# Kernel tuning notes

Hardware: AMD Instinct MI355X
Metric: run time of the kernel (lower is better)

## Reference

```python
import jax, jax.numpy as jnp
import numpy as np

N = 50000      # nodes
E = 800000     # edges (before self-loops)
DIN = 146      # input feature dim
D = 128        # hidden/out dim
G = 64         # graphs in batch
L = 4          # number of GCNConv layers (len(hidden_dims[1:]) + 1)
NC = 10        # classes
EPS = 1e-5     # BatchNorm eps


def setup_inputs() -> dict:
    key = jax.random.key(0)
    ks = jax.random.split(key, 12)
    x = jax.random.normal(ks[0], (N, DIN), jnp.float32)
    edge_index = jax.random.randint(ks[1], (2, E), 0, N, dtype=jnp.int64)
    batch = jnp.sort(jax.random.randint(ks[2], (N,), 0, G, dtype=jnp.int64))

    def lin(k, shape, fan_in):
        return (jax.random.normal(k, shape, jnp.float32) / np.sqrt(fan_in)).astype(jnp.float32)

    W_emb = lin(ks[3], (DIN, D), DIN)
    b_emb = jnp.zeros((D,), jnp.float32)
    W_gcn = lin(ks[4], (L, D, D), D)
    b_gcn = jnp.zeros((L, D), jnp.float32)
    bn_gamma = jnp.ones((L, D), jnp.float32)
    bn_beta = jnp.zeros((L, D), jnp.float32)
    W_r1 = lin(ks[5], (D, D // 2), D)
    b_r1 = jnp.zeros((D // 2,), jnp.float32)
    W_r2 = lin(ks[6], (D // 2, D // 4), D // 2)
    b_r2 = jnp.zeros((D // 4,), jnp.float32)
    W_r3 = lin(ks[7], (D // 4, NC), D // 4)
    b_r3 = jnp.zeros((NC,), jnp.float32)
    return {"x": x, "edge_index": edge_index, "batch": batch,
            "W_emb": W_emb, "b_emb": b_emb, "W_gcn": W_gcn, "b_gcn": b_gcn,
            "bn_gamma": bn_gamma, "bn_beta": bn_beta,
            "W_r1": W_r1, "b_r1": b_r1, "W_r2": W_r2, "b_r2": b_r2,
            "W_r3": W_r3, "b_r3": b_r3}


def reference(x, edge_index, batch, W_emb, b_emb, W_gcn, b_gcn,
              bn_gamma, bn_beta, W_r1, b_r1, W_r2, b_r2, W_r3, b_r3):
    # gcn_norm with self-loops (fill_value=1, improved=False)
    loop = jnp.arange(N, dtype=edge_index.dtype)
    src = jnp.concatenate([edge_index[0], loop])
    dst = jnp.concatenate([edge_index[1], loop])
    deg = jax.ops.segment_sum(jnp.ones(src.shape, x.dtype), dst, num_segments=N)
    dinv = jax.lax.rsqrt(jnp.maximum(deg, jnp.asarray(1e-12, x.dtype)))  # deg >= 1 (self loops)
    norm = (dinv[src] * dinv[dst])[:, None]  # [E+N, 1]

    h = x @ W_emb + b_emb  # embedding_h
    for l in range(L):
        h_in = h
        m = h @ W_gcn[l]                                            # [N, D]
        h = jax.ops.segment_sum(m[src] * norm, dst, num_segments=N) + b_gcn[l]
        # BatchNorm1d (training-mode batch stats, biased var)
        mu = h.mean(axis=0)
        var = h.var(axis=0)
        h = (h - mu) * jax.lax.rsqrt(var + EPS) * bn_gamma[l] + bn_beta[l]
        h = jax.nn.relu(h)
        h = h_in + h  # residual (dims always match here)

    # global_mean_pool over batch ids
    sums = jax.ops.segment_sum(h, batch, num_segments=G)
    cnts = jax.ops.segment_sum(jnp.ones((N, 1), h.dtype), batch, num_segments=G)
    hg = sums / jnp.maximum(cnts, 1.0)

    # MLPReadout: two hidden layers halving dims, then classifier
    z = jax.nn.relu(hg @ W_r1 + b_r1)
    z = jax.nn.relu(z @ W_r2 + b_r2)
    return z @ W_r3 + b_r3  # [G, NC]
```

## Files before the change

kernel.cpp:

```cpp
#include <hip/hip_runtime.h>
#include <hip/hip_bf16.h>

#define NN 50000
#define EE 800000
#define DIN 146
#define DD 128
#define GG 64
#define LL 4
#define NC 10
#define BN_EPS 1e-5f

#define KP_EMB 160
#define AST_L  136
#define NCOPY 64
#define NPW 4
#define RST 129

#define C_INIT   256
#define C_REPACK (C_INIT + 31250)
#define C_BATCH  (C_REPACK + 196)
#define C_PARAMS (C_BATCH + 384)
#define C_WT     (C_PARAMS + 400)

#define B_EDGE 3125
#define B_TOT  (B_EDGE + 391)
#define S_SCAT 3125
#define S_TOT  (S_SCAT + 391)

typedef __attribute__((ext_vector_type(8))) short bf16x8;
typedef __attribute__((ext_vector_type(4))) float f32x4;

__device__ __forceinline__ float bf2f(__hip_bfloat16 v) { return __bfloat162float(v); }
__device__ __forceinline__ float loadf(const void* p, long i, int f32) {
    return f32 ? ((const float*)p)[i] : bf2f(((const __hip_bfloat16*)p)[i]);
}
__device__ __forceinline__ unsigned short f2bf_bits(float f) {
    __hip_bfloat16 h = __float2bfloat16(f);
    return *(unsigned short*)&h;
}
__device__ __forceinline__ float bfu2f(unsigned short u) {
    return __uint_as_float((unsigned)u << 16);
}
__device__ __forceinline__ void acc_add8(float* acc, uint4 v) {
    acc[0] += __uint_as_float(v.x << 16);
    acc[1] += __uint_as_float(v.x & 0xffff0000u);
    acc[2] += __uint_as_float(v.y << 16);
    acc[3] += __uint_as_float(v.y & 0xffff0000u);
    acc[4] += __uint_as_float(v.z << 16);
    acc[5] += __uint_as_float(v.z & 0xffff0000u);
    acc[6] += __uint_as_float(v.w << 16);
    acc[7] += __uint_as_float(v.w & 0xffff0000u);
}

__global__ void detect_kernel(const void* ei, const void* batch, const void* Wemb,
                              int* __restrict__ flags) {
    __shared__ int s_edge_nz, s_batch_nz, s_f32_cnt;
    int t = threadIdx.x;
    if (t == 0) { s_edge_nz = 0; s_batch_nz = 0; s_f32_cnt = 0; }
    __syncthreads();
    {   const int* w = (const int*)ei;
        long j = ((long)t * ((2L * EE) / 64)) | 1;
        if (w[j] != 0) atomicAdd(&s_edge_nz, 1);
    }
    {   const int* w = (const int*)batch;
        long j = ((long)(NN / 2) + (long)t * ((NN / 2) / 64)) | 1;
        if (j < NN && w[j] != 0) atomicAdd(&s_batch_nz, 1);
    }
    {   const unsigned short* w = (const unsigned short*)Wemb;
        unsigned short v = w[2 * t];
        int ex = (v >> 7) & 0xFF;
        if (v != 0 && ex >= 128) atomicAdd(&s_f32_cnt, 1);
    }
    __syncthreads();
    if (t == 0) {
        flags[0] = (s_edge_nz == 0) ? 1 : 0;
        flags[1] = (s_batch_nz == 0) ? 1 : 0;
        flags[2] = (s_f32_cnt >= 8) ? 1 : 0;
    }
}

struct Param { const void* src; float* dst; int src_n; int dst_n; };
struct Params12 { Param p[12]; };
struct WtDesc { const void* src; long src_off; unsigned short* dst; int K; int Kpad; };
struct WtDescs5 { WtDesc p[5]; };

__global__ __launch_bounds__(256) void mega_conv_kernel(
    const void* __restrict__ x, const void* __restrict__ batch,
    const int* __restrict__ flags, unsigned short* __restrict__ xb,
    int* __restrict__ deg, float* __restrict__ statmulti, float* __restrict__ hgsum,
    int* __restrict__ b32, Params12 P, WtDescs5 W)
{
    int b = blockIdx.x;
    int t = threadIdx.x;
    if (b < C_INIT) {
        int i = b * 256 + t;
        if (i < NN) deg[i] = 0;
        if (i < LL * NCOPY * 256) statmulti[i] = 0.0f;
        if (i < GG * DD) hgsum[i] = 0.0f;
    } else if (b < C_REPACK) {
        int f32 = flags[2];
        long idx = (long)(b - C_INIT) * 256 + t;
        int row = (int)(idx / KP_EMB);
        int k = (int)(idx - (long)row * KP_EMB);
        float v = (k < DIN) ? loadf(x, (long)row * DIN + k, f32) : 0.0f;
        xb[idx] = f2bf_bits(v);
    } else if (b < C_BATCH) {
        int i = (b - C_REPACK) * 256 + t;
        if (i < NN) b32[i] = flags[1] ? ((const int*)batch)[2L * i] : ((const int*)batch)[i];
    } else if (b < C_PARAMS) {
        int f32 = flags[2];
        int bb = b - C_BATCH;
        const Param& e = P.p[bb >> 5];
        int idx = (bb & 31) * 256 + t;
        if (idx < e.dst_n)
            e.dst[idx] = (idx < e.src_n) ? loadf(e.src, idx, f32) : 0.0f;
    } else {
        int f32 = flags[2];
        int bb = b - C_PARAMS;
        int y = bb / 80;
        const WtDesc& e = W.p[y];
        int idx = (bb - y * 80) * 256 + t;
        if (idx < 128 * e.Kpad) {
            int n = idx / e.Kpad, k = idx - n * e.Kpad;
            float v = (k < e.K) ? loadf(e.src, e.src_off + (long)k * DD + n, f32) : 0.0f;
            e.dst[idx] = f2bf_bits(v);
        }
    }
}


__global__ __launch_bounds__(256) void edge_emb_kernel(
    const void* __restrict__ ei, const int* __restrict__ flags,
    int* __restrict__ src32, int* __restrict__ dst32,
    int* __restrict__ rank, int* __restrict__ deg,
    const unsigned short* __restrict__ Ab,
    const unsigned short* __restrict__ Wt,
    const float* __restrict__ bias,
    unsigned short* __restrict__ hb, int n)
{
    int t = threadIdx.x;
    if (blockIdx.x < B_EDGE) {
        int e = blockIdx.x * 256 + t;
        const int* w = (const int*)ei;
        int s, d;
        if (flags[0]) { s = w[2L * e]; d = w[2L * (EE + e)]; }
        else          { s = w[e];      d = w[EE + e]; }
        src32[e] = s; dst32[e] = d;
        int r = 0;
        if ((unsigned)d < (unsigned)NN) r = atomicAdd(&deg[d], 1);
        rank[e] = r;
        return;
    }
    int r0 = (blockIdx.x - B_EDGE) * 128;
    int lane = t & 63, w = t >> 6;
    int m = lane & 15, quad = lane >> 4;
    int rbase = r0 + w * 32;
    bf16x8 a[2][5];
    #pragma unroll
    for (int rt = 0; rt < 2; ++rt)
        #pragma unroll
        for (int c = 0; c < 5; ++c) {
            int rr = rbase + rt * 16 + m; if (rr > n - 1) rr = n - 1;
            a[rt][c] = *(const bf16x8*)(Ab + (long)rr * KP_EMB + c * 32 + quad * 8);
        }
    f32x4 acc[2][8];
    #pragma unroll
    for (int t8 = 0; t8 < 8; ++t8) {
        float bv = bias[t8 * 16 + m];
        f32x4 ai = {bv, bv, bv, bv};
        acc[0][t8] = ai; acc[1][t8] = ai;
    }
    #pragma unroll
    for (int t8 = 0; t8 < 8; ++t8) {
        #pragma unroll
        for (int c = 0; c < 5; ++c) {
            bf16x8 b = *(const bf16x8*)(Wt + (long)(t8 * 16 + m) * KP_EMB + c * 32 + quad * 8);
            acc[0][t8] = __builtin_amdgcn_mfma_f32_16x16x32_bf16(a[0][c], b, acc[0][t8], 0, 0, 0);
            acc[1][t8] = __builtin_amdgcn_mfma_f32_16x16x32_bf16(a[1][c], b, acc[1][t8], 0, 0, 0);
        }
    }
    #pragma unroll
    for (int rt = 0; rt < 2; ++rt)
        #pragma unroll
        for (int t8 = 0; t8 < 8; ++t8)
            #pragma unroll
            for (int rg = 0; rg < 4; ++rg) {
                int row = rbase + rt * 16 + quad * 4 + rg;
                int col = t8 * 16 + m;
                if (row < n) hb[(long)row * DD + col] = f2bf_bits(acc[rt][t8][rg]);
            }
}

__global__ void scan1_kernel(const int* __restrict__ cnt, int* __restrict__ off,
                             int* __restrict__ bsum, float* __restrict__ dinv, int n) {
    int t = threadIdx.x;
    int i = blockIdx.x * 256 + t;
    int v = (i < n) ? cnt[i] : 0;
    if (i < n) dinv[i] = rsqrtf((float)(v + 1));
    int lane = t & 63, w = t >> 6;
    int x = v;
    #pragma unroll
    for (int s = 1; s < 64; s <<= 1) {
        int y = __shfl_up(x, s, 64);
        if (lane >= s) x += y;
    }
    __shared__ int wsum[4];
    if (lane == 63) wsum[w] = x;
    __syncthreads();
    if (t == 0) {
        int a = 0;
        #pragma unroll
        for (int k = 0; k < 4; ++k) { int tmp = wsum[k]; wsum[k] = a; a += tmp; }
        bsum[blockIdx.x] = a;
    }
    __syncthreads();
    int excl = x - v + wsum[w];
    if (i < n) off[i] = excl;
}

__global__ void scan2_kernel(int* __restrict__ bsum, int* __restrict__ boff,
                             int* __restrict__ off_last, int nb) {
    int t = threadIdx.x;
    int v = (t < nb) ? bsum[t] : 0;
    int lane = t & 63, w = t >> 6;
    int x = v;
    #pragma unroll
    for (int s = 1; s < 64; s <<= 1) {
        int y = __shfl_up(x, s, 64);
        if (lane >= s) x += y;
    }
    __shared__ int wsum[4];
    if (lane == 63) wsum[w] = x;
    __syncthreads();
    __shared__ int total_s;
    if (t == 0) {
        int a = 0;
        #pragma unroll
        for (int k = 0; k < 4; ++k) { int tmp = wsum[k]; wsum[k] = a; a += tmp; }
        total_s = a;
    }
    __syncthreads();
    int bval = x - v + wsum[w];
    if (t < nb) boff[t] = bval;
    if (t == nb - 1) *off_last = total_s - bval;
}

__global__ __launch_bounds__(256) void scat_mm_kernel(
    const int* __restrict__ src, const int* __restrict__ dst,
    const int* __restrict__ rank, const int* __restrict__ off,
    const int* __restrict__ boff, int* __restrict__ src_s,
    const unsigned short* __restrict__ Ab,
    const unsigned short* __restrict__ Wt,
    const float* __restrict__ dinv,
    unsigned short* __restrict__ Mb, int n)
{
    int t = threadIdx.x;
    if (blockIdx.x < S_SCAT) {
        int e = blockIdx.x * 256 + t;
        int s = src[e], d = dst[e];
        if ((unsigned)s >= (unsigned)NN || (unsigned)d >= (unsigned)NN) return;
        src_s[off[d] + boff[d >> 8] + rank[e]] = s;
        return;
    }
    int r0 = (blockIdx.x - S_SCAT) * 128;
    int lane = t & 63, w = t >> 6;
    int m = lane & 15, quad = lane >> 4;
    int rbase = r0 + w * 32;
    bf16x8 a[2][4];
    #pragma unroll
    for (int rt = 0; rt < 2; ++rt)
        #pragma unroll
        for (int c = 0; c < 4; ++c) {
            int rr = rbase + rt * 16 + m; if (rr > n - 1) rr = n - 1;
            a[rt][c] = *(const bf16x8*)(Ab + (long)rr * DD + c * 32 + quad * 8);
        }
    float dv[2][4];
    #pragma unroll
    for (int rt = 0; rt < 2; ++rt)
        #pragma unroll
        for (int rg = 0; rg < 4; ++rg) {
            int row = rbase + rt * 16 + quad * 4 + rg; if (row > n - 1) row = n - 1;
            dv[rt][rg] = dinv[row];
        }
    f32x4 acc[2][8];
    #pragma unroll
    for (int t8 = 0; t8 < 8; ++t8) {
        f32x4 z = {0.f, 0.f, 0.f, 0.f};
        acc[0][t8] = z; acc[1][t8] = z;
    }
    #pragma unroll
    for (int t8 = 0; t8 < 8; ++t8) {
        #pragma unroll
        for (int c = 0; c < 4; ++c) {
            bf16x8 b = *(const bf16x8*)(Wt + (long)(t8 * 16 + m) * DD + c * 32 + quad * 8);
            acc[0][t8] = __builtin_amdgcn_mfma_f32_16x16x32_bf16(a[0][c], b, acc[0][t8], 0, 0, 0);
            acc[1][t8] = __builtin_amdgcn_mfma_f32_16x16x32_bf16(a[1][c], b, acc[1][t8], 0, 0, 0);
        }
    }
    #pragma unroll
    for (int rt = 0; rt < 2; ++rt)
        #pragma unroll
        for (int t8 = 0; t8 < 8; ++t8)
            #pragma unroll
            for (int rg = 0; rg < 4; ++rg) {
                int row = rbase + rt * 16 + quad * 4 + rg;
                int col = t8 * 16 + m;
                if (row < n) Mb[(long)row * DD + col] = f2bf_bits(dv[rt][rg] * acc[rt][t8][rg]);
            }
}

__global__ __launch_bounds__(256) void gemm_fused_kernel(
    const unsigned short* __restrict__ aggb, unsigned short* __restrict__ hb,
    const float* __restrict__ statmulti, const float* __restrict__ gamma,
    const float* __restrict__ beta, const float* __restrict__ dinv,
    const unsigned short* __restrict__ Wt, unsigned short* __restrict__ Mb, int n)
{
    __shared__ unsigned short As[128 * AST_L];
    __shared__ float bnsh[256];
    int t = threadIdx.x;
    int r0 = blockIdx.x * 128;
    {
        float s = 0.0f;
        #pragma unroll 8
        for (int k = 0; k < NCOPY; ++k) s += statmulti[k * 256 + t];
        bnsh[t] = s;
    }
    __syncthreads();
    {
        int c4 = (t & 31) * 4, rsub = t >> 5;
        float inv_n = 1.0f / (float)n;
        float4 sm = *(const float4*)&bnsh[c4];
        float4 sq = *(const float4*)&bnsh[128 + c4];
        float4 ga = *(const float4*)&gamma[c4];
        float4 be = *(const float4*)&beta[c4];
        float4 mu, rs;
        mu.x = sm.x * inv_n; mu.y = sm.y * inv_n; mu.z = sm.z * inv_n; mu.w = sm.w * inv_n;
        rs.x = rsqrtf(sq.x * inv_n - mu.x * mu.x + BN_EPS) * ga.x;
        rs.y = rsqrtf(sq.y * inv_n - mu.y * mu.y + BN_EPS) * ga.y;
        rs.z = rsqrtf(sq.z * inv_n - mu.z * mu.z + BN_EPS) * ga.z;
        rs.w = rsqrtf(sq.w * inv_n - mu.w * mu.w + BN_EPS) * ga.w;
        #pragma unroll 4
        for (int i = 0; i < 16; ++i) {
            int row = i * 8 + rsub;
            int r = r0 + row;
            unsigned short o0 = 0, o1 = 0, o2 = 0, o3 = 0;
            if (r < n) {
                long g = (long)r * DD + c4;
                ushort4 au = *(const ushort4*)&aggb[g];
                ushort4 hu = *(const ushort4*)&hb[g];
                float h0 = bfu2f(hu.x) + fmaxf((bfu2f(au.x) - mu.x) * rs.x + be.x, 0.0f);
                float h1 = bfu2f(hu.y) + fmaxf((bfu2f(au.y) - mu.y) * rs.y + be.y, 0.0f);
                float h2 = bfu2f(hu.z) + fmaxf((bfu2f(au.z) - mu.z) * rs.z + be.z, 0.0f);
                float h3 = bfu2f(hu.w) + fmaxf((bfu2f(au.w) - mu.w) * rs.w + be.w, 0.0f);
                o0 = f2bf_bits(h0); o1 = f2bf_bits(h1);
                o2 = f2bf_bits(h2); o3 = f2bf_bits(h3);
                ushort4 ho; ho.x = o0; ho.y = o1; ho.z = o2; ho.w = o3;
                *(ushort4*)&hb[g] = ho;
            }
            unsigned short* dst = &As[row * AST_L + c4];
            dst[0] = o0; dst[1] = o1; dst[2] = o2; dst[3] = o3;
        }
    }
    __syncthreads();
    int lane = t & 63, w = t >> 6;
    int m = lane & 15, quad = lane >> 4;
    int rl = w * 32;
    int rbase = r0 + rl;
    bf16x8 a[2][4];
    #pragma unroll
    for (int rt = 0; rt < 2; ++rt)
        #pragma unroll
        for (int c = 0; c < 4; ++c)
            a[rt][c] = *(const bf16x8*)(As + (rl + rt * 16 + m) * AST_L + c * 32 + quad * 8);
    float dv[2][4];
    #pragma unroll
    for (int rt = 0; rt < 2; ++rt)
        #pragma unroll
        for (int rg = 0; rg < 4; ++rg) {
            int row = rbase + rt * 16 + quad * 4 + rg; if (row > n - 1) row = n - 1;
            dv[rt][rg] = dinv[row];
        }
    f32x4 acc[2][8];
    #pragma unroll
    for (int t8 = 0; t8 < 8; ++t8) {
        f32x4 z = {0.f, 0.f, 0.f, 0.f};
        acc[0][t8] = z; acc[1][t8] = z;
    }
    #pragma unroll
    for (int t8 = 0; t8 < 8; ++t8) {
        #pragma unroll
        for (int c = 0; c < 4; ++c) {
            bf16x8 b = *(const bf16x8*)(Wt + (long)(t8 * 16 + m) * DD + c * 32 + quad * 8);
            acc[0][t8] = __builtin_amdgcn_mfma_f32_16x16x32_bf16(a[0][c], b, acc[0][t8], 0, 0, 0);
            acc[1][t8] = __builtin_amdgcn_mfma_f32_16x16x32_bf16(a[1][c], b, acc[1][t8], 0, 0, 0);
        }
    }
    #pragma unroll
    for (int rt = 0; rt < 2; ++rt)
        #pragma unroll
        for (int t8 = 0; t8 < 8; ++t8)
            #pragma unroll
            for (int rg = 0; rg < 4; ++rg) {
                int row = rbase + rt * 16 + quad * 4 + rg;
                int col = t8 * 16 + m;
                if (row < n) Mb[(long)row * DD + col] = f2bf_bits(dv[rt][rg] * acc[rt][t8][rg]);
            }
}

__global__ __launch_bounds__(256) void agg_kernel(
    const unsigned short* __restrict__ mb, const int* __restrict__ off,
    const int* __restrict__ boff, const int* __restrict__ src_s,
    const float* __restrict__ dinv, const float* __restrict__ bias,
    unsigned short* __restrict__ aggb, float* __restrict__ statacc)
{
    __shared__ float sred[4][4 * RST];
    __shared__ float2 ssum[4][64], ssq[4][64];
    int t = threadIdx.x;
    int wv = t >> 6, lane = t & 63;
    int grp = lane >> 4, sl = lane & 15;
    float* red = sred[wv];
    float2 bi = ((const float2*)bias)[lane];
    float2 sAcc = {0.0f, 0.0f}, qAcc = {0.0f, 0.0f};
    int i0 = (blockIdx.x * 4 + wv) * NPW;
    #pragma unroll 1
    for (int ni = 0; ni < NPW; ++ni) {
        int i = i0 + ni;
        if (i >= NN) break;
        float acc[8];
        #pragma unroll
        for (int k = 0; k < 8; ++k) acc[k] = 0.0f;
        if (grp == 0) {
            uint4 v = *(const uint4*)(mb + (long)i * DD + sl * 8);
            acc_add8(acc, v);
        }
        int e  = off[i] + boff[i >> 8];
        int e1 = off[i + 1] + boff[(i + 1) >> 8];
        for (; e + 16 <= e1; e += 16) {
            int j0 = src_s[e + grp];
            int j1 = src_s[e + 4 + grp];
            int j2 = src_s[e + 8 + grp];
            int j3 = src_s[e + 12 + grp];
            uint4 v0 = *(const uint4*)(mb + (long)j0 * DD + sl * 8);
            uint4 v1 = *(const uint4*)(mb + (long)j1 * DD + sl * 8);
            uint4 v2 = *(const uint4*)(mb + (long)j2 * DD + sl * 8);
            uint4 v3 = *(const uint4*)(mb + (long)j3 * DD + sl * 8);
            acc_add8(acc, v0);
            acc_add8(acc, v1);
            acc_add8(acc, v2);
            acc_add8(acc, v3);
        }
        for (; e + 8 <= e1; e += 8) {
            int ja = src_s[e + grp];
            int jb = src_s[e + 4 + grp];
            uint4 va = *(const uint4*)(mb + (long)ja * DD + sl * 8);
            uint4 vb = *(const uint4*)(mb + (long)jb * DD + sl * 8);
            acc_add8(acc, va);
            acc_add8(acc, vb);
        }
        for (; e + 4 <= e1; e += 4) {
            int j = src_s[e + grp];
            uint4 v = *(const uint4*)(mb + (long)j * DD + sl * 8);
            acc_add8(acc, v);
        }
        if (e + grp < e1) {
            int j = src_s[e + grp];
            uint4 v = *(const uint4*)(mb + (long)j * DD + sl * 8);
            acc_add8(acc, v);
        }
        #pragma unroll
        for (int k = 0; k < 8; ++k) red[grp * RST + sl * 8 + k] = acc[k];
        asm volatile("" ::: "memory");
        float c0 = 0.0f, c1 = 0.0f;
        #pragma unroll
        for (int g = 0; g < 4; ++g) {
            c0 += red[g * RST + 2 * lane];
            c1 += red[g * RST + 2 * lane + 1];
        }
        asm volatile("" ::: "memory");
        float di = dinv[i];
        float o0 = di * c0 + bi.x;
        float o1 = di * c1 + bi.y;
        unsigned packed = ((unsigned)f2bf_bits(o1) << 16) | f2bf_bits(o0);
        ((unsigned*)aggb)[(long)i * 64 + lane] = packed;
        sAcc.x += o0; sAcc.y += o1;
        qAcc.x += o0 * o0; qAcc.y += o1 * o1;
    }
    ssum[wv][lane] = sAcc; ssq[wv][lane] = qAcc;
    __syncthreads();
    if (wv == 0) {
        float2 s0 = ssum[0][lane], s1 = ssum[1][lane], s2 = ssum[2][lane], s3 = ssum[3][lane];
        float2 q0 = ssq[0][lane], q1 = ssq[1][lane], q2 = ssq[2][lane], q3 = ssq[3][lane];
        float sx = s0.x + s1.x + s2.x + s3.x;
        float sy = s0.y + s1.y + s2.y + s3.y;
        float qx = q0.x + q1.x + q2.x + q3.x;
        float qy = q0.y + q1.y + q2.y + q3.y;
        float* copy = statacc + (blockIdx.x & (NCOPY - 1)) * 256;
        atomicAdd(&copy[2 * lane], sx);
        atomicAdd(&copy[2 * lane + 1], sy);
        atomicAdd(&copy[128 + 2 * lane], qx);
        atomicAdd(&copy[128 + 2 * lane + 1], qy);
    }
}

__global__ void pool1_kernel(const unsigned short* __restrict__ hb,
                             const unsigned short* __restrict__ aggb,
                             const float* __restrict__ statmulti,
                             const float* __restrict__ gamma, const float* __restrict__ beta,
                             const int* __restrict__ b32, float* __restrict__ hgsum, int n) {
    __shared__ float bnsh[256];
    int t = threadIdx.x;
    {
        float s = 0.0f;
        #pragma unroll 8
        for (int k = 0; k < NCOPY; ++k) s += statmulti[k * 256 + t];
        bnsh[t] = s;
    }
    __syncthreads();
    int c4 = (t & 31) * 4, rsub = t >> 5;
    float inv_n = 1.0f / (float)n;
    float4 sm = *(const float4*)&bnsh[c4];
    float4 sq = *(const float4*)&bnsh[128 + c4];
    float4 ga = *(const float4*)&gamma[c4];
    float4 be = *(const float4*)&beta[c4];
    float4 mu, rs;
    mu.x = sm.x * inv_n; mu.y = sm.y * inv_n; mu.z = sm.z * inv_n; mu.w = sm.w * inv_n;
    rs.x = rsqrtf(sq.x * inv_n - mu.x * mu.x + BN_EPS) * ga.x;
    rs.y = rsqrtf(sq.y * inv_n - mu.y * mu.y + BN_EPS) * ga.y;
    rs.z = rsqrtf(sq.z * inv_n - mu.z * mu.z + BN_EPS) * ga.z;
    rs.w = rsqrtf(sq.w * inv_n - mu.w * mu.w + BN_EPS) * ga.w;
    int rows_pb = (n + gridDim.x - 1) / gridDim.x;
    int r0 = blockIdx.x * rows_pb;
    int r1 = min(n, r0 + rows_pb);
    float4 acc = {0, 0, 0, 0};
    int gcur = -1;
    for (int r = r0 + rsub; r < r1; r += 8) {
        int g = b32[r];
        if (g != gcur) {
            if (gcur >= 0) {
                atomicAdd(&hgsum[gcur * DD + c4 + 0], acc.x);
                atomicAdd(&hgsum[gcur * DD + c4 + 1], acc.y);
                atomicAdd(&hgsum[gcur * DD + c4 + 2], acc.z);
                atomicAdd(&hgsum[gcur * DD + c4 + 3], acc.w);
            }
            acc.x = acc.y = acc.z = acc.w = 0.0f;
            gcur = ((unsigned)g < (unsigned)GG) ? g : -1;
        }
        if (gcur >= 0) {
            long ix = (long)r * DD + c4;
            ushort4 au = *(const ushort4*)&aggb[ix];
            ushort4 hu = *(const ushort4*)&hb[ix];
            acc.x += bfu2f(hu.x) + fmaxf((bfu2f(au.x) - mu.x) * rs.x + be.x, 0.0f);
            acc.y += bfu2f(hu.y) + fmaxf((bfu2f(au.y) - mu.y) * rs.y + be.y, 0.0f);
            acc.z += bfu2f(hu.z) + fmaxf((bfu2f(au.z) - mu.z) * rs.z + be.z, 0.0f);
            acc.w += bfu2f(hu.w) + fmaxf((bfu2f(au.w) - mu.w) * rs.w + be.w, 0.0f);
        }
    }
    if (gcur >= 0) {
        atomicAdd(&hgsum[gcur * DD + c4 + 0], acc.x);
        atomicAdd(&hgsum[gcur * DD + c4 + 1], acc.y);
        atomicAdd(&hgsum[gcur * DD + c4 + 2], acc.z);
        atomicAdd(&hgsum[gcur * DD + c4 + 3], acc.w);
    }
}

__device__ int lower_bound_i(const int* __restrict__ a, int n, int v) {
    int lo = 0, hi = n;
    while (lo < hi) {
        int mid = (lo + hi) >> 1;
        if (a[mid] < v) lo = mid + 1; else hi = mid;
    }
    return lo;
}

__global__ void readout_kernel(const float* __restrict__ hgsum, const int* __restrict__ b32,
                               const float* __restrict__ W1, const float* __restrict__ b1,
                               const float* __restrict__ W2, const float* __restrict__ b2,
                               const float* __restrict__ W3, const float* __restrict__ b3,
                               const int* __restrict__ flags, void* __restrict__ out, int n) {
    int f32 = flags[2];
    int g = blockIdx.x;
    int t = threadIdx.x;
    __shared__ float hgs[DD];
    __shared__ float z1[DD / 2];
    __shared__ float z2[DD / 4];
    int lo = lower_bound_i(b32, n, g);
    int hi = lower_bound_i(b32, n, g + 1);
    float invc = 1.0f / fmaxf((float)(hi - lo), 1.0f);
    hgs[t] = hgsum[g * DD + t] * invc;
    __syncthreads();
    if (t < DD / 2) {
        float acc = b1[t];
        #pragma unroll 8
        for (int k = 0; k < DD; ++k) acc = fmaf(hgs[k], W1[k * (DD / 2) + t], acc);
        z1[t] = fmaxf(acc, 0.0f);
    }
    __syncthreads();
    if (t < DD / 4) {
        float acc = b2[t];
        #pragma unroll 8
        for (int k = 0; k < DD / 2; ++k) acc = fmaf(z1[k], W2[k * (DD / 4) + t], acc);
        z2[t] = fmaxf(acc, 0.0f);
    }
    __syncthreads();
    if (t < NC) {
        float acc = b3[t];
        #pragma unroll 8
        for (int k = 0; k < DD / 4; ++k) acc = fmaf(z2[k], W3[k * NC + t], acc);
        if (f32) ((float*)out)[g * NC + t] = acc;
        else     ((__hip_bfloat16*)out)[g * NC + t] = __float2bfloat16(acc);
    }
}

extern "C" void kernel_launch(void* const* d_in, const int* in_sizes, int n_in,
                              void* d_out, int out_size, void* d_ws, size_t ws_size,
                              hipStream_t stream) {
    const void* x      = d_in[0];
    const void* ei     = d_in[1];
    const void* batch  = d_in[2];
    const void* W_emb  = d_in[3];
    const void* b_emb  = d_in[4];
    const void* W_gcn  = d_in[5];
    const void* b_gcn  = d_in[6];
    const void* bn_g   = d_in[7];
    const void* bn_b   = d_in[8];
    const void* W_r1   = d_in[9];
    const void* b_r1   = d_in[10];
    const void* W_r2   = d_in[11];
    const void* b_r2   = d_in[12];
    const void* W_r3   = d_in[13];
    const void* b_r3   = d_in[14];

    char* p = (char*)d_ws;
    auto alloc = [&](size_t bytes) -> void* {
        void* r = (void*)p;
        p += (bytes + 255) & ~(size_t)255;
        return r;
    };
    int*   flags  = (int*)alloc(64 * 4);
    int*   deg    = (int*)alloc((size_t)NN * 4);
    float* statmulti = (float*)alloc((size_t)LL * NCOPY * 256 * 4);
    float* hgsum  = (float*)alloc((size_t)GG * DD * 4);
    int*   off    = (int*)alloc((size_t)(NN + 1) * 4);
    float* dinv   = (float*)alloc((size_t)NN * 4);
    int*   src32  = (int*)alloc((size_t)EE * 4);
    int*   dst32  = (int*)alloc((size_t)EE * 4);
    int*   rank   = (int*)alloc((size_t)EE * 4);
    int*   b32    = (int*)alloc((size_t)NN * 4);
    int*   src_s  = (int*)alloc((size_t)EE * 4);
    int*   bsum   = (int*)alloc(256 * 4);
    int*   boff   = (int*)alloc(256 * 4);
    unsigned short* hb = (unsigned short*)alloc((size_t)NN * DD * 2);
    unsigned short* mb = (unsigned short*)alloc((size_t)NN * DD * 2);
    unsigned short* aggb = (unsigned short*)alloc((size_t)NN * DD * 2);
    unsigned short* xb = (unsigned short*)alloc((size_t)NN * KP_EMB * 2);
    unsigned short* wt_emb = (unsigned short*)alloc((size_t)DD * KP_EMB * 2);
    unsigned short* wt_gcn = (unsigned short*)alloc((size_t)LL * DD * DD * 2);
    float* b_emb32 = (float*)alloc(DD * 4);
    float* b_gcn32 = (float*)alloc((size_t)LL * DD * 4);
    float* bng32   = (float*)alloc((size_t)LL * DD * 4);
    float* bnb32   = (float*)alloc((size_t)LL * DD * 4);
    float* wr1     = (float*)alloc((size_t)DD * (DD / 2) * 4);
    float* br1     = (float*)alloc((DD / 2) * 4);
    float* wr2     = (float*)alloc((size_t)(DD / 2) * (DD / 4) * 4);
    float* br2     = (float*)alloc((DD / 4) * 4);
    float* wr3     = (float*)alloc((size_t)(DD / 4) * NC * 4);
    float* br3     = (float*)alloc(NC * 4);

    detect_kernel<<<1, 64, 0, stream>>>(ei, batch, W_emb, flags);

    Params12 P;
    P.p[0]  = { b_emb, b_emb32, DD, DD };
    P.p[1]  = { b_gcn, b_gcn32, LL * DD, LL * DD };
    P.p[2]  = { bn_g,  bng32,   LL * DD, LL * DD };
    P.p[3]  = { bn_b,  bnb32,   LL * DD, LL * DD };
    P.p[4]  = { W_r1,  wr1,     DD * (DD / 2), DD * (DD / 2) };
    P.p[5]  = { b_r1,  br1,     DD / 2, DD / 2 };
    P.p[6]  = { W_r2,  wr2,     (DD / 2) * (DD / 4), (DD / 2) * (DD / 4) };
    P.p[7]  = { b_r2,  br2,     DD / 4, DD / 4 };
    P.p[8]  = { W_r3,  wr3,     (DD / 4) * NC, (DD / 4) * NC };
    P.p[9]  = { b_r3,  br3,     NC, NC };
    P.p[10] = { b_r3,  br3,     0, 0 };
    P.p[11] = { b_r3,  br3,     0, 0 };

    WtDescs5 W;
    W.p[0] = { W_emb, 0,            wt_emb,                DIN, KP_EMB };
    W.p[1] = { W_gcn, 0L * DD * DD, wt_gcn + 0L * DD * DD, DD,  DD };
    W.p[2] = { W_gcn, 1L * DD * DD, wt_gcn + 1L * DD * DD, DD,  DD };
    W.p[3] = { W_gcn, 2L * DD * DD, wt_gcn + 2L * DD * DD, DD,  DD };
    W.p[4] = { W_gcn, 3L * DD * DD, wt_gcn + 3L * DD * DD, DD,  DD };

    mega_conv_kernel<<<C_WT, 256, 0, stream>>>(x, batch, flags, xb, deg, statmulti,
                                               hgsum, b32, P, W);

    edge_emb_kernel<<<B_TOT, 256, 0, stream>>>(ei, flags, src32, dst32, rank, deg,
                                               xb, wt_emb, b_emb32, hb, NN);

    int nb = (NN + 255) / 256;
    scan1_kernel<<<nb, 256, 0, stream>>>(deg, off, bsum, dinv, NN);
    scan2_kernel<<<1, 256, 0, stream>>>(bsum, boff, off + NN, nb);

    scat_mm_kernel<<<S_TOT, 256, 0, stream>>>(src32, dst32, rank, off, boff, src_s,
                                              hb, wt_gcn, dinv, mb, NN);

    int ngemm = (NN + 127) / 128;
    int nagg = (NN + 4 * NPW - 1) / (4 * NPW);
    for (int l = 0; l < LL; ++l) {
        if (l > 0) {
            gemm_fused_kernel<<<ngemm, 256, 0, stream>>>(
                aggb, hb, statmulti + (size_t)(l - 1) * NCOPY * 256,
                bng32 + (l - 1) * DD, bnb32 + (l - 1) * DD,
                dinv, wt_gcn + (size_t)l * DD * DD, mb, NN);
        }
        agg_kernel<<<nagg, 256, 0, stream>>>(mb, off, boff, src_s, dinv,
                                             b_gcn32 + l * DD, aggb,
                                             statmulti + (size_t)l * NCOPY * 256);
    }

    pool1_kernel<<<512, 256, 0, stream>>>(hb, aggb, statmulti + (size_t)(LL - 1) * NCOPY * 256,
                                          bng32 + (LL - 1) * DD, bnb32 + (LL - 1) * DD,
                                          b32, hgsum, NN);
    readout_kernel<<<GG, DD, 0, stream>>>(hgsum, b32, wr1, br1, wr2, br2, wr3, br3,
                                          flags, d_out, NN);
}
```

Measured before the change: 436.4 us.

## Swap MFMA operands for vectorized row stores and vectorize edge preprocessing

Swaps the A/B operands of the MFMA calls so each lane holds four consecutive output columns of one row. This lets the GEMM epilogues write 8-byte ushort4 stores instead of scattered 2-byte stores, and cuts the per-row dinv loads from eight to two. The edge-processing blocks now handle four edges per thread with int4 loads and stores, and are placed after the GEMM blocks in the grid. This reduces the number of memory transactions. The trade-off is more register pressure and some added complexity in the index handling.

```diff
diff --git a/kernel.cpp b/kernel.cpp
--- a/kernel.cpp
+++ b/kernel.cpp
@@ -22,10 +22,9 @@
 #define C_PARAMS (C_BATCH + 384)
 #define C_WT     (C_PARAMS + 400)
 
-#define B_EDGE 3125
-#define B_TOT  (B_EDGE + 391)
-#define S_SCAT 3125
-#define S_TOT  (S_SCAT + 391)
+#define B_GEMM 391
+#define B_EDGE 782
+#define B_TOT  (B_GEMM + B_EDGE)
 
 typedef __attribute__((ext_vector_type(8))) short bf16x8;
 typedef __attribute__((ext_vector_type(4))) float f32x4;
@@ -50,6 +49,18 @@
     acc[5] += __uint_as_float(v.z & 0xffff0000u);
     acc[6] += __uint_as_float(v.w << 16);
     acc[7] += __uint_as_float(v.w & 0xffff0000u);
+}
+__device__ __forceinline__ ushort4 pack4(f32x4 v) {
+    ushort4 u;
+    u.x = f2bf_bits(v[0]); u.y = f2bf_bits(v[1]);
+    u.z = f2bf_bits(v[2]); u.w = f2bf_bits(v[3]);
+    return u;
+}
+__device__ __forceinline__ ushort4 pack4s(f32x4 v, float s) {
+    ushort4 u;
+    u.x = f2bf_bits(s * v[0]); u.y = f2bf_bits(s * v[1]);
+    u.z = f2bf_bits(s * v[2]); u.w = f2bf_bits(s * v[3]);
+    return u;
 }
 
 __global__ void detect_kernel(const void* ei, const void* batch, const void* Wemb,
@@ -139,19 +150,33 @@
     unsigned short* __restrict__ hb, int n)
 {
     int t = threadIdx.x;
-    if (blockIdx.x < B_EDGE) {
-        int e = blockIdx.x * 256 + t;
+    if (blockIdx.x >= B_GEMM) {
+        int e0 = ((blockIdx.x - B_GEMM) * 256 + t) * 4;
+        if (e0 >= EE) return;
         const int* w = (const int*)ei;
-        int s, d;
-        if (flags[0]) { s = w[2L * e]; d = w[2L * (EE + e)]; }
-        else          { s = w[e];      d = w[EE + e]; }
-        src32[e] = s; dst32[e] = d;
-        int r = 0;
-        if ((unsigned)d < (unsigned)NN) r = atomicAdd(&deg[d], 1);
-        rank[e] = r;
+        int4 sv, dv;
+        if (flags[0]) {
+            int4 u0 = *(const int4*)(w + 2L * e0);
+            int4 u1 = *(const int4*)(w + 2L * e0 + 4);
+            int4 v0 = *(const int4*)(w + 2L * (EE + e0));
+            int4 v1 = *(const int4*)(w + 2L * (EE + e0) + 4);
+            sv = make_int4(u0.x, u0.z, u1.x, u1.z);
+            dv = make_int4(v0.x, v0.z, v1.x, v1.z);
+        } else {
+            sv = *(const int4*)(w + e0);
+            dv = *(const int4*)(w + EE + e0);
+        }
+        *(int4*)(src32 + e0) = sv;
+        *(int4*)(dst32 + e0) = dv;
+        int4 rv = make_int4(0, 0, 0, 0);
+        if ((unsigned)dv.x < (unsigned)NN) rv.x = atomicAdd(&deg[dv.x], 1);
+        if ((unsigned)dv.y < (unsigned)NN) rv.y = atomicAdd(&deg[dv.y], 1);
+        if ((unsigned)dv.z < (unsigned)NN) rv.z = atomicAdd(&deg[dv.z], 1);
+        if ((unsigned)dv.w < (unsigned)NN) rv.w = atomicAdd(&deg[dv.w], 1);
+        *(int4*)(rank + e0) = rv;
         return;
     }
-    int r0 = (blockIdx.x - B_EDGE) * 128;
+    int r0 = blockIdx.x * 128;
     int lane = t & 63, w = t >> 6;
     int m = lane & 15, quad = lane >> 4;
     int rbase = r0 + w * 32;
@@ -166,8 +191,8 @@
     f32x4 acc[2][8];
     #pragma unroll
     for (int t8 = 0; t8 < 8; ++t8) {
-        float bv = bias[t8 * 16 + m];
-        f32x4 ai = {bv, bv, bv, bv};
+        float4 bv = *(const float4*)&bias[t8 * 16 + quad * 4];
+        f32x4 ai = {bv.x, bv.y, bv.z, bv.w};
         acc[0][t8] = ai; acc[1][t8] = ai;
     }
     #pragma unroll
@@ -175,20 +200,19 @@
         #pragma unroll
         for (int c = 0; c < 5; ++c) {
             bf16x8 b = *(const bf16x8*)(Wt + (long)(t8 * 16 + m) * KP_EMB + c * 32 + quad * 8);
-            acc[0][t8] = __builtin_amdgcn_mfma_f32_16x16x32_bf16(a[0][c], b, acc[0][t8], 0, 0, 0);
-            acc[1][t8] = __builtin_amdgcn_mfma_f32_16x16x32_bf16(a[1][c], b, acc[1][t8], 0, 0, 0);
-        }
-    }
-    #pragma unroll
-    for (int rt = 0; rt < 2; ++rt)
-        #pragma unroll
-        for (int t8 = 0; t8 < 8; ++t8)
+            acc[0][t8] = __builtin_amdgcn_mfma_f32_16x16x32_bf16(b, a[0][c], acc[0][t8], 0, 0, 0);
+            acc[1][t8] = __builtin_amdgcn_mfma_f32_16x16x32_bf16(b, a[1][c], acc[1][t8], 0, 0, 0);
+        }
+    }
+    #pragma unroll
+    for (int rt = 0; rt < 2; ++rt) {
+        int row = rbase + rt * 16 + m;
+        if (row < n) {
             #pragma unroll
-            for (int rg = 0; rg < 4; ++rg) {
-                int row = rbase + rt * 16 + quad * 4 + rg;
-                int col = t8 * 16 + m;
-                if (row < n) hb[(long)row * DD + col] = f2bf_bits(acc[rt][t8][rg]);
-            }
+            for (int t8 = 0; t8 < 8; ++t8)
+                *(ushort4*)(hb + (long)row * DD + t8 * 16 + quad * 4) = pack4(acc[rt][t8]);
+        }
+    }
 }
 
 __global__ void scan1_kernel(const int* __restrict__ cnt, int* __restrict__ off,
@@ -255,14 +279,29 @@
     unsigned short* __restrict__ Mb, int n)
 {
     int t = threadIdx.x;
-    if (blockIdx.x < S_SCAT) {
-        int e = blockIdx.x * 256 + t;
-        int s = src[e], d = dst[e];
-        if ((unsigned)s >= (unsigned)NN || (unsigned)d >= (unsigned)NN) return;
-        src_s[off[d] + boff[d >> 8] + rank[e]] = s;
+    if (blockIdx.x >= B_GEMM) {
+        int e0 = ((blockIdx.x - B_GEMM) * 256 + t) * 4;
+        if (e0 >= EE) return;
+        int4 sv = *(const int4*)(src + e0);
+        int4 dv = *(const int4*)(dst + e0);
+        int4 rv = *(const int4*)(rank + e0);
+        int ss[4] = {sv.x, sv.y, sv.z, sv.w};
+        int dd2[4] = {dv.x, dv.y, dv.z, dv.w};
+        int rr[4] = {rv.x, rv.y, rv.z, rv.w};
+        int pos[4];
+        #pragma unroll
+        for (int k = 0; k < 4; ++k) {
+            int d = dd2[k];
+            int dcl = ((unsigned)d < (unsigned)NN) ? d : 0;
+            pos[k] = off[dcl] + boff[dcl >> 8] + rr[k];
+        }
+        #pragma unroll
+        for (int k = 0; k < 4; ++k)
+            if ((unsigned)dd2[k] < (unsigned)NN && (unsigned)ss[k] < (unsigned)NN)
+                src_s[pos[k]] = ss[k];
         return;
     }
-    int r0 = (blockIdx.x - S_SCAT) * 128;
+    int r0 = blockIdx.x * 128;
     int lane = t & 63, w = t >> 6;
     int m = lane & 15, quad = lane >> 4;
     int rbase = r0 + w * 32;
@@ -274,14 +313,15 @@
             int rr = rbase + rt * 16 + m; if (rr > n - 1) rr = n - 1;
             a[rt][c] = *(const bf16x8*)(Ab + (long)rr * DD + c * 32 + quad * 8);
         }
-    float dv[2][4];
-    #pragma unroll
-    for (int rt = 0; rt < 2; ++rt)
-        #pragma unroll
-        for (int rg = 0; rg < 4; ++rg) {
-            int row = rbase + rt * 16 + quad * 4 + rg; if (row > n - 1) row = n - 1;
-            dv[rt][rg] = dinv[row];
-        }
+    float dvt[2];
+    int rowt[2];
+    #pragma unroll
+    for (int rt = 0; rt < 2; ++rt) {
+        int rr = rbase + rt * 16 + m;
+        rowt[rt] = rr;
+        if (rr > n - 1) rr = n - 1;
+        dvt[rt] = dinv[rr];
+    }
     f32x4 acc[2][8];
     #pragma unroll
     for (int t8 = 0; t8 < 8; ++t8) {
@@ -293,20 +333,18 @@
         #pragma unroll
         for (int c = 0; c < 4; ++c) {
             bf16x8 b = *(const bf16x8*)(Wt + (long)(t8 * 16 + m) * DD + c * 32 + quad * 8);
-            acc[0][t8] = __builtin_amdgcn_mfma_f32_16x16x32_bf16(a[0][c], b, acc[0][t8], 0, 0, 0);
-            acc[1][t8] = __builtin_amdgcn_mfma_f32_16x16x32_bf16(a[1][c], b, acc[1][t8], 0, 0, 0);
-        }
-    }
-    #pragma unroll
-    for (int rt = 0; rt < 2; ++rt)
-        #pragma unroll
-        for (int t8 = 0; t8 < 8; ++t8)
+            acc[0][t8] = __builtin_amdgcn_mfma_f32_16x16x32_bf16(b, a[0][c], acc[0][t8], 0, 0, 0);
+            acc[1][t8] = __builtin_amdgcn_mfma_f32_16x16x32_bf16(b, a[1][c], acc[1][t8], 0, 0, 0);
+        }
+    }
+    #pragma unroll
+    for (int rt = 0; rt < 2; ++rt) {
+        if (rowt[rt] < n) {
             #pragma unroll
-            for (int rg = 0; rg < 4; ++rg) {
-                int row = rbase + rt * 16 + quad * 4 + rg;
-                int col = t8 * 16 + m;
-                if (row < n) Mb[(long)row * DD + col] = f2bf_bits(dv[rt][rg] * acc[rt][t8][rg]);
-            }
+            for (int t8 = 0; t8 < 8; ++t8)
+                *(ushort4*)(Mb + (long)rowt[rt] * DD + t8 * 16 + quad * 4) = pack4s(acc[rt][t8], dvt[rt]);
+        }
+    }
 }
 
 __global__ __launch_bounds__(256) void gemm_fused_kernel(
@@ -372,14 +410,15 @@
         #pragma unroll
         for (int c = 0; c < 4; ++c)
             a[rt][c] = *(const bf16x8*)(As + (rl + rt * 16 + m) * AST_L + c * 32 + quad * 8);
-    float dv[2][4];
-    #pragma unroll
-    for (int rt = 0; rt < 2; ++rt)
-        #pragma unroll
-        for (int rg = 0; rg < 4; ++rg) {
-            int row = rbase + rt * 16 + quad * 4 + rg; if (row > n - 1) row = n - 1;
-            dv[rt][rg] = dinv[row];
-        }
+    float dvt[2];
+    int rowt[2];
+    #pragma unroll
+    for (int rt = 0; rt < 2; ++rt) {
+        int rr = rbase + rt * 16 + m;
+        rowt[rt] = rr;
+        if (rr > n - 1) rr = n - 1;
+        dvt[rt] = dinv[rr];
+    }
     f32x4 acc[2][8];
     #pragma unroll
     for (int t8 = 0; t8 < 8; ++t8) {
@@ -391,20 +430,18 @@
         #pragma unroll
         for (int c = 0; c < 4; ++c) {
             bf16x8 b = *(const bf16x8*)(Wt + (long)(t8 * 16 + m) * DD + c * 32 + quad * 8);
-            acc[0][t8] = __builtin_amdgcn_mfma_f32_16x16x32_bf16(a[0][c], b, acc[0][t8], 0, 0, 0);
-            acc[1][t8] = __builtin_amdgcn_mfma_f32_16x16x32_bf16(a[1][c], b, acc[1][t8], 0, 0, 0);
-        }
-    }
-    #pragma unroll
-    for (int rt = 0; rt < 2; ++rt)
-        #pragma unroll
-        for (int t8 = 0; t8 < 8; ++t8)
+            acc[0][t8] = __builtin_amdgcn_mfma_f32_16x16x32_bf16(b, a[0][c], acc[0][t8], 0, 0, 0);
+            acc[1][t8] = __builtin_amdgcn_mfma_f32_16x16x32_bf16(b, a[1][c], acc[1][t8], 0, 0, 0);
+        }
+    }
+    #pragma unroll
+    for (int rt = 0; rt < 2; ++rt) {
+        if (rowt[rt] < n) {
             #pragma unroll
-            for (int rg = 0; rg < 4; ++rg) {
-                int row = rbase + rt * 16 + quad * 4 + rg;
-                int col = t8 * 16 + m;
-                if (row < n) Mb[(long)row * DD + col] = f2bf_bits(dv[rt][rg] * acc[rt][t8][rg]);
-            }
+            for (int t8 = 0; t8 < 8; ++t8)
+                *(ushort4*)(Mb + (long)rowt[rt] * DD + t8 * 16 + quad * 4) = pack4s(acc[rt][t8], dvt[rt]);
+        }
+    }
 }
 
 __global__ __launch_bounds__(256) void agg_kernel(
@@ -699,7 +736,7 @@
     scan1_kernel<<<nb, 256, 0, stream>>>(deg, off, bsum, dinv, NN);
     scan2_kernel<<<1, 256, 0, stream>>>(bsum, boff, off + NN, nb);
 
-    scat_mm_kernel<<<S_TOT, 256, 0, stream>>>(src32, dst32, rank, off, boff, src_s,
+    scat_mm_kernel<<<B_TOT, 256, 0, stream>>>(src32, dst32, rank, off, boff, src_s,
                                               hb, wt_gcn, dinv, mb, NN);
 
     int ngemm = (NN + 127) / 128;
```

Result: no change. 429.0 us (-1.7%).
